# Kernel tuning notes

Measured on AMD Instinct MI355X. Metric: run time of the kernel, lower is better.

Reference implementation:

```python
import jax, jax.numpy as jnp
import jax.scipy.linalg as jsl
import numpy as np

B, T, C = 2, 4096, 1024
HK = HV = 8           # linear_num_key_heads == linear_num_value_heads
DK = DV = 128         # linear_key_head_dim / linear_value_head_dim
CHUNK = 64
CONV_K = 4
KEY_DIM = HK * DK
VAL_DIM = HV * DV
CONV_DIM = 2 * KEY_DIM + VAL_DIM
EPS = 1e-6


def setup_inputs() -> dict:
    key = jax.random.key(0)
    ks = jax.random.split(key, 8)
    s = 0.02
    x = jax.random.normal(ks[0], (B, T, C), jnp.float32)
    W_qkvz = jax.random.normal(ks[1], (C, 2 * KEY_DIM + 2 * VAL_DIM), jnp.float32) * s
    W_ba = jax.random.normal(ks[2], (C, 2 * HV), jnp.float32) * s
    conv_w = jax.random.normal(ks[3], (CONV_DIM, 1, CONV_K), jnp.float32) * 0.3  # depthwise (O,1,K)
    dt_bias = jnp.ones((HV,), jnp.float32)
    A_log = jnp.log(jax.random.uniform(ks[4], (HV,), jnp.float32, 0.5, 8.0))
    norm_weight = jnp.ones((DV,), jnp.float32)
    W_out = jax.random.normal(ks[5], (VAL_DIM, C), jnp.float32) * s
    return {"x": x, "W_qkvz": W_qkvz, "W_ba": W_ba, "conv_w": conv_w,
            "dt_bias": dt_bias, "A_log": A_log, "norm_weight": norm_weight, "W_out": W_out}


def _l2norm(x, eps=EPS):
    return x * jax.lax.rsqrt(jnp.sum(x * x, -1, keepdims=True) + eps)


def _chunk_gated_delta_rule(q, k, v, g, beta, chunk=CHUNK):
    # q,k: (B,T,H,DK); v: (B,T,H,DV); g,beta: (B,T,H)
    q = _l2norm(q)
    k = _l2norm(k)
    tr = lambda x: jnp.swapaxes(x, 1, 2).astype(jnp.float32)  # -> (B,H,T,...)
    q, k, v, g, beta = tr(q), tr(k), tr(v), tr(g), tr(beta)
    b, h, t, dk = k.shape
    dv = v.shape[-1]
    n = t // chunk  # T divisible by chunk (pad_size == 0)
    q = q * (dk ** -0.5)
    v_beta = v * beta[..., None]
    k_beta = k * beta[..., None]
    rs = lambda x: x.reshape(b, h, n, chunk, x.shape[-1])
    q, k, v_beta, k_beta = rs(q), rs(k), rs(v_beta), rs(k_beta)
    g = jnp.cumsum(g.reshape(b, h, n, chunk), axis=-1)
    # decay_mask[..., i, j] = exp(g_i - g_j) for j <= i, else 0
    decay = jnp.tril(jnp.exp(jnp.tril(g[..., :, None] - g[..., None, :])))
    # forward substitution == unit-lower-triangular solve: (I + tri)^{-1}
    tri = jnp.tril(jnp.einsum('bhnck,bhndk->bhncd', k_beta, k) * decay, -1)
    eye = jnp.eye(chunk, dtype=jnp.float32)
    Tm = jsl.solve_triangular(eye + tri, jnp.broadcast_to(eye, tri.shape), lower=True)
    v_new = Tm @ v_beta                                   # (B,H,N,C,DV)
    k_cum = Tm @ (k_beta * jnp.exp(g)[..., None])         # (B,H,N,C,DK)
    keep_low = jnp.tril(jnp.ones((chunk, chunk), bool))

    def step(S, inp):
        q_i, k_i, v_i, kc_i, g_i, dm_i = inp              # (B,H,C,*)
        attn = jnp.where(keep_low, (q_i @ jnp.swapaxes(k_i, -1, -2)) * dm_i, 0.0)
        v_n = v_i - kc_i @ S
        out = (q_i * jnp.exp(g_i)[..., None]) @ S + attn @ v_n
        g_last = g_i[..., -1]
        S = S * jnp.exp(g_last)[..., None, None] + jnp.einsum(
            'bhck,bhcv->bhkv', k_i * jnp.exp(g_last[..., None] - g_i)[..., None], v_n)
        return S, out

    mv = lambda x: jnp.moveaxis(x, 2, 0)                  # chunk axis to front
    S0 = jnp.zeros((b, h, dk, dv), jnp.float32)
    S, outs = jax.lax.scan(step, S0, (mv(q), mv(k), mv(v_new), mv(k_cum), mv(g), mv(decay)))
    out = jnp.moveaxis(outs, 0, 2).reshape(b, h, t, dv)
    return jnp.swapaxes(out, 1, 2), S                     # (B,T,H,DV), (B,H,DK,DV)


def reference(x, W_qkvz, W_ba, conv_w, dt_bias, A_log, norm_weight, W_out):
    Bx, Tx, Cx = x.shape
    ratio = HV // HK
    qkvz = (x @ W_qkvz).reshape(Bx, Tx, HK, 2 * DK + 2 * ratio * DV)
    q, k, v, z = jnp.split(qkvz, [DK, 2 * DK, 2 * DK + ratio * DV], axis=3)
    v = v.reshape(Bx, Tx, HV, DV)
    z = z.reshape(Bx, Tx, HV, DV)
    ba = (x @ W_ba).reshape(Bx, Tx, HK, 2 * ratio)
    b_, a_ = jnp.split(ba, [ratio], axis=3)
    b_ = b_.reshape(Bx, Tx, HV)
    a_ = a_.reshape(Bx, Tx, HV)
    mixed = jnp.concatenate([q.reshape(Bx, Tx, -1), k.reshape(Bx, Tx, -1),
                             v.reshape(Bx, Tx, -1)], axis=-1)
    # causal depthwise conv1d (left pad K-1, take first T)
    xc = jnp.swapaxes(mixed, 1, 2)                        # (B, CONV_DIM, T)
    conv = jax.lax.conv_general_dilated(xc, conv_w, (1,), [(CONV_K - 1, 0)],
                                        dimension_numbers=('NCH', 'OIH', 'NCH'),
                                        feature_group_count=CONV_DIM)
    conv = jnp.swapaxes(jax.nn.silu(conv), 1, 2)          # (B,T,CONV_DIM)
    qc, kc, vc = jnp.split(conv, [KEY_DIM, 2 * KEY_DIM], axis=-1)
    qc = qc.reshape(Bx, Tx, HK, DK)
    kc = kc.reshape(Bx, Tx, HK, DK)
    vc = vc.reshape(Bx, Tx, HV, DV)
    if ratio > 1:
        qc = jnp.repeat(qc, ratio, axis=2)
        kc = jnp.repeat(kc, ratio, axis=2)
    beta = jax.nn.sigmoid(b_)
    g = -jnp.exp(A_log) * jax.nn.softplus(a_ + dt_bias)
    core, _ = _chunk_gated_delta_rule(qc, kc, vc, g, beta)
    # GatedRMSNorm over head_v_dim, gated by silu(z)
    h = core.astype(jnp.float32)
    var = jnp.mean(h * h, -1, keepdims=True)
    h = norm_weight * (h * jax.lax.rsqrt(var + EPS))
    h = h * jax.nn.silu(z.astype(jnp.float32))
    return h.reshape(Bx, Tx, VAL_DIM) @ W_out
```

## Files before the change

kernel.cpp:

```cpp
#include <hip/hip_runtime.h>
#include <cstddef>

#define Bx 2
#define Tn 4096
#define Hh 8

typedef unsigned short u16;
typedef unsigned int u32;
typedef __attribute__((ext_vector_type(8))) short short8;
typedef __attribute__((ext_vector_type(4))) float f32x4;

__device__ __forceinline__ float bf2f(u16 u) {
  u32 x = ((u32)u) << 16;
  return __uint_as_float(x);
}
__device__ __forceinline__ u16 f2bf(float f) {
  u32 x = __float_as_uint(f);
  u32 lsb = (x >> 16) & 1;
  x += 0x7fffu + lsb;
  return (u16)(x >> 16);
}
__device__ __forceinline__ u32 pack2(float a, float b) {
  return (u32)f2bf(a) | ((u32)f2bf(b) << 16);
}
__device__ __forceinline__ short8 cvt8(float4 f0, float4 f1) {
  uint4 p;
  p.x = pack2(f0.x, f0.y);
  p.y = pack2(f0.z, f0.w);
  p.z = pack2(f1.x, f1.y);
  p.w = pack2(f1.z, f1.w);
  return *(short8*)&p;
}
__device__ __forceinline__ void async16(u16* lds, const u16* g) {
  __builtin_amdgcn_global_load_lds((const __attribute__((address_space(1))) void*)g,
                                   (__attribute__((address_space(3))) void*)lds, 16, 0, 0);
}

__global__ __launch_bounds__(256) void conv_bf16(const float* __restrict__ X,
                                                 u16* __restrict__ Xb) {
  int i = (blockIdx.x * 256 + threadIdx.x) * 8;
  float4 v0 = *(const float4*)&X[i];
  float4 v1 = *(const float4*)&X[i + 4];
  uint4 pv;
  pv.x = pack2(v0.x, v0.y);
  pv.y = pack2(v0.z, v0.w);
  pv.z = pack2(v1.x, v1.y);
  pv.w = pack2(v1.z, v1.w);
  *(uint4*)&Xb[i] = pv;
}

__global__ __launch_bounds__(256) void transpose_bf16(const float* __restrict__ W,
                                                      u16* __restrict__ WT,
                                                      int K, int N) {
  __shared__ float tile[64][68];
  int nb = blockIdx.x, kb = blockIdx.y;
  int tid = threadIdx.x;
  int r = tid >> 4, c4 = (tid & 15) * 4;
#pragma unroll
  for (int p = 0; p < 4; p++) {
    int k = kb * 64 + p * 16 + r;
    float4 v = *(const float4*)&W[(size_t)k * N + nb * 64 + c4];
    tile[p * 16 + r][c4] = v.x;
    tile[p * 16 + r][c4 + 1] = v.y;
    tile[p * 16 + r][c4 + 2] = v.z;
    tile[p * 16 + r][c4 + 3] = v.w;
  }
  __syncthreads();
  int rn = tid >> 2, ck = (tid & 3) * 16;
#pragma unroll
  for (int s = 0; s < 2; s++) {
    int k0 = ck + s * 8;
    uint4 pv;
    pv.x = pack2(tile[k0 + 0][rn], tile[k0 + 1][rn]);
    pv.y = pack2(tile[k0 + 2][rn], tile[k0 + 3][rn]);
    pv.z = pack2(tile[k0 + 4][rn], tile[k0 + 5][rn]);
    pv.w = pack2(tile[k0 + 6][rn], tile[k0 + 7][rn]);
    *(uint4*)&WT[(size_t)(nb * 64 + rn) * K + kb * 64 + k0] = pv;
  }
}

template<int EPI>
__global__ __launch_bounds__(256) void gemm_mfma(const u16* __restrict__ A,
                                                 const u16* __restrict__ Bt,
                                                 u16* __restrict__ O1,
                                                 u16* __restrict__ O2,
                                                 float* __restrict__ O3,
                                                 int Nfull) {
  const int K = 1024;
  __shared__ u16 As[128 * 32];
  __shared__ u16 Bs[128 * 32];
  int bn = blockIdx.x, bm = blockIdx.y;
  int tid = threadIdx.x;
  int wave = tid >> 6, lane = tid & 63;
  int wr = wave >> 1, wc = wave & 1;

  f32x4 acc[4][4];
#pragma unroll
  for (int i = 0; i < 4; i++)
#pragma unroll
    for (int j = 0; j < 4; j++) acc[i][j] = (f32x4){0.f, 0.f, 0.f, 0.f};

  const u16* Ab = A + (size_t)(bm * 128 + wave * 32 + (lane >> 2)) * K + (lane & 3) * 8;
  const u16* Bb = Bt + (size_t)(bn * 128 + wave * 32 + (lane >> 2)) * K + (lane & 3) * 8;
  u16* AsW = &As[(wave * 32) * 32];
  u16* BsW = &Bs[(wave * 32) * 32];

  int m_lane = lane & 15, k_lane = (lane >> 4) * 8;
  const u16* arow0 = &As[(wr * 64 + m_lane) * 32 + k_lane];
  const u16* brow0 = &Bs[(wc * 64 + m_lane) * 32 + k_lane];

  for (int kk = 0; kk < K; kk += 32) {
    __syncthreads();
    async16(AsW, Ab + kk);
    async16(AsW + 16 * 32, Ab + 16 * K + kk);
    async16(BsW, Bb + kk);
    async16(BsW + 16 * 32, Bb + 16 * K + kk);
    __syncthreads();
    short8 a[4], b[4];
#pragma unroll
    for (int t = 0; t < 4; t++) a[t] = *(const short8*)(arow0 + t * 16 * 32);
#pragma unroll
    for (int t = 0; t < 4; t++) b[t] = *(const short8*)(brow0 + t * 16 * 32);
#pragma unroll
    for (int i = 0; i < 4; i++)
#pragma unroll
      for (int j = 0; j < 4; j++)
        acc[i][j] = __builtin_amdgcn_mfma_f32_16x16x32_bf16(a[i], b[j], acc[i][j], 0, 0, 0);
  }

  int n0 = bn * 128;
  int cbase = wc * 64 + (lane & 15);
  int rbase = bm * 128 + wr * 64 + ((lane >> 4) * 4);
  if (EPI == 1) {
    int h = n0 >> 9, sub = (n0 >> 7) & 3;
    u16* dst;
    size_t stride;
    if (sub < 3) { dst = O1 + (size_t)(sub * 1024 + h * 128); stride = 3072; }
    else         { dst = O2 + (size_t)(h * 128);              stride = 1024; }
#pragma unroll
    for (int i = 0; i < 4; i++)
#pragma unroll
      for (int j = 0; j < 4; j++)
#pragma unroll
        for (int r = 0; r < 4; r++)
          dst[(size_t)(rbase + i * 16 + r) * stride + cbase + j * 16] = f2bf(acc[i][j][r]);
  } else {
#pragma unroll
    for (int i = 0; i < 4; i++)
#pragma unroll
      for (int j = 0; j < 4; j++)
#pragma unroll
        for (int r = 0; r < 4; r++)
          O3[(size_t)(rbase + i * 16 + r) * Nfull + n0 + cbase + j * 16] = acc[i][j][r];
  }
}

__global__ __launch_bounds__(128) void ba_kernel(const float* __restrict__ x,
                                                 const float* __restrict__ Wba,
                                                 const float* __restrict__ dtb,
                                                 const float* __restrict__ Alog,
                                                 float* __restrict__ betab,
                                                 float* __restrict__ gb) {
  __shared__ float xs[1024];
  __shared__ float part[8][16];
  int row = blockIdx.x, tid = threadIdx.x;
#pragma unroll
  for (int r = 0; r < 2; r++) {
    int f4 = r * 128 + tid;
    *(float4*)&xs[f4 * 4] = *(const float4*)&x[(size_t)row * 1024 + f4 * 4];
  }
  __syncthreads();
  int col = tid & 15, seg = tid >> 4;
  float a = 0.f;
  for (int k = seg * 128; k < seg * 128 + 128; k++) a += xs[k] * Wba[k * 16 + col];
  part[seg][col] = a;
  __syncthreads();
  if (tid < 8) {
    float bval = 0.f, aval = 0.f;
#pragma unroll
    for (int q = 0; q < 8; q++) { bval += part[q][tid * 2]; aval += part[q][tid * 2 + 1]; }
    betab[(size_t)row * 8 + tid] = 1.f / (1.f + expf(-bval));
    float spin = aval + dtb[tid];
    float sp = (spin > 20.f) ? spin : log1pf(expf(spin));
    gb[(size_t)row * 8 + tid] = -expf(Alog[tid]) * sp;
  }
}

__global__ __launch_bounds__(256) void convnorm(const u16* __restrict__ mixed,
                                                const float* __restrict__ cw,
                                                const float* __restrict__ gbuf,
                                                u16* __restrict__ qn,
                                                u16* __restrict__ kn,
                                                u16* __restrict__ kdT) {
  __shared__ __align__(16) u16 sRaw[67 * 128];
  __shared__ __align__(16) u16 sO[64 * 136];
  __shared__ float red_s[256];
  __shared__ float inv_s[64];
  __shared__ float eglc_s[64];
  int n = blockIdx.x, bh = blockIdx.y, type = blockIdx.z;
  int b = bh >> 3, h = bh & 7;
  int t0 = n * 64, tid = threadIdx.x;
  int srow = tid >> 4, scol8 = (tid & 15) * 8;
  int base = type * 1024;

#pragma unroll
  for (int pass = 0; pass < 5; pass++) {
    int r = pass * 16 + srow;
    if (r < 67) {
      int t = t0 - 3 + r;
      uint4 v = make_uint4(0u, 0u, 0u, 0u);
      if (t >= 0) v = *(const uint4*)&mixed[(size_t)(b * Tn + t) * 3072 + base + h * 128 + scol8];
      *(uint4*)&sRaw[r * 128 + scol8] = v;
    }
  }
  if (type == 1 && tid < 64) {
    float gv = gbuf[(size_t)(b * Tn + t0 + tid) * 8 + h];
#pragma unroll
    for (int off = 1; off < 64; off <<= 1) {
      float o = __shfl_up(gv, off, 64);
      if (tid >= off) gv += o;
    }
    float gl = __shfl(gv, 63, 64);
    eglc_s[tid] = expf(gl - gv);
  }
  __syncthreads();

#pragma unroll
  for (int it = 0; it < 32; it++) {
    int idx = it * 256 + tid;
    int i = idx >> 7, d = idx & 127;
    int colw = (base + h * 128 + d) * 4;
    float a = 0.f;
#pragma unroll
    for (int tap = 0; tap < 4; tap++)
      a += bf2f(sRaw[(i + tap) * 128 + d]) * cw[colw + tap];
    a = a / (1.f + expf(-a));
    sO[i * 136 + d] = f2bf(a);
  }
  __syncthreads();
  {
    int i = tid >> 2, p = tid & 3;
    float ss = 0.f;
#pragma unroll
    for (int d = p * 32; d < p * 32 + 32; d += 2) {
      u32 w2 = *(const u32*)&sO[i * 136 + d];
      float a = bf2f(w2 & 0xffff), b2 = bf2f(w2 >> 16);
      ss += a * a + b2 * b2;
    }
    red_s[tid] = ss;
  }
  __syncthreads();
  if (tid < 64) {
    float inv = rsqrtf(red_s[tid * 4] + red_s[tid * 4 + 1] + red_s[tid * 4 + 2] + red_s[tid * 4 + 3] + 1e-6f);
    inv_s[tid] = (type == 0) ? inv * 0.08838834764831845f : inv;
  }
  __syncthreads();
  u16* dstRow = (type == 0 ? qn : kn) + (size_t)(bh * Tn + t0) * 128;
#pragma unroll
  for (int it = 0; it < 16; it++) {
    int idx = it * 256 + tid;
    int i = idx >> 6, d2 = (idx & 63) * 2;
    u32 w2 = *(const u32*)&sO[i * 136 + d2];
    float inv = inv_s[i];
    float q0 = bf2f(w2 & 0xffff) * inv, q1 = bf2f(w2 >> 16) * inv;
    u32 pk = pack2(q0, q1);
    if (type == 1) *(u32*)&sO[i * 136 + d2] = pk;
    *(u32*)&dstRow[(size_t)i * 128 + d2] = pk;
  }
  if (type == 1) {
    __syncthreads();
    const size_t tbase = (size_t)(bh * 64 + n) * 8192;
#pragma unroll
    for (int it = 0; it < 32; it++) {
      int idx = it * 256 + tid;
      int d = idx >> 6, i = idx & 63;
      kdT[tbase + d * 64 + i] = f2bf(bf2f(sO[i * 136 + d]) * eglc_s[i]);
    }
  }
}

__global__ __launch_bounds__(256) void prep(const u16* __restrict__ mixed,
                                            const float* __restrict__ cw,
                                            const float* __restrict__ gbuf,
                                            const float* __restrict__ betabuf,
                                            u16* qbuf,
                                            u16* kbuf,
                                            u16* __restrict__ vnT,
                                            u16* __restrict__ attn,
                                            float* __restrict__ egl) {
  __shared__ __align__(16) u16 sKn[64 * 136];
  __shared__ __align__(16) u16 sQn[64 * 136];
  __shared__ __align__(16) u16 sRawV[67 * 128];
  __shared__ float gc_s[64], egc_s[64], bet_s[64];
  float* triL = (float*)sQn;

  int n = blockIdx.x, bh = blockIdx.y;
  int b = bh >> 3, h = bh & 7;
  int t0 = n * 64;
  int tid = threadIdx.x;
  const int rowg0 = b * Tn + t0;
  const int rowh0 = bh * Tn + t0;
  const size_t tbase = (size_t)(bh * 64 + n) * 8192;

  int wv = tid >> 6, lane = tid & 63;
  int m16 = lane & 15, q8 = (lane >> 4) * 8, qr = (lane >> 4) * 4;
  int srow = tid >> 4, scol8 = (tid & 15) * 8;

#pragma unroll
  for (int it = 0; it < 4; it++) {
    int idx = it * 256 + tid;
    int i = idx >> 4, c8 = (idx & 15) * 8;
    *(uint4*)&sQn[i * 136 + c8] = *(const uint4*)&qbuf[(size_t)(rowh0 + i) * 128 + c8];
    *(uint4*)&sKn[i * 136 + c8] = *(const uint4*)&kbuf[(size_t)(rowh0 + i) * 128 + c8];
  }
#pragma unroll
  for (int pass = 0; pass < 5; pass++) {
    int r = pass * 16 + srow;
    if (r < 67) {
      int t = t0 - 3 + r;
      uint4 v = make_uint4(0u, 0u, 0u, 0u);
      if (t >= 0) v = *(const uint4*)&mixed[(size_t)(b * Tn + t) * 3072 + 2048 + h * 128 + scol8];
      *(uint4*)&sRawV[r * 128 + scol8] = v;
    }
  }
  if (tid < 64) {
    float gv = gbuf[(size_t)(rowg0 + tid) * 8 + h];
    float bv = betabuf[(size_t)(rowg0 + tid) * 8 + h];
#pragma unroll
    for (int off = 1; off < 64; off <<= 1) {
      float o = __shfl_up(gv, off, 64);
      if (tid >= off) gv += o;
    }
    float gl = __shfl(gv, 63, 64);
    gc_s[tid] = gv;
    egc_s[tid] = expf(gv);
    bet_s[tid] = bv;
    if (tid == 63) egl[bh * 64 + n] = expf(gl);
  }
  __syncthreads();

#pragma unroll
  for (int it = 0; it < 16; it++) {
    int idx = it * 256 + tid;
    int i = idx >> 6, d2 = (idx & 63) * 2;
    u32 w2 = *(const u32*)&sQn[i * 136 + d2];
    float e = egc_s[i];
    *(u32*)&qbuf[(size_t)(rowh0 + i) * 128 + d2] =
        pack2(bf2f(w2 & 0xffff) * e, bf2f(w2 >> 16) * e);
  }
  {
    short8 qa[4];
#pragma unroll
    for (int kt = 0; kt < 4; kt++)
      qa[kt] = *(const short8*)&sQn[(wv * 16 + m16) * 136 + kt * 32 + q8];
    u16* atp = attn + (size_t)(bh * 64 + n) * 4096;
#pragma unroll
    for (int jt = 0; jt < 4; jt++) {
      int j = jt * 16 + m16;
      if (jt <= wv) {
        f32x4 o = (f32x4){0.f, 0.f, 0.f, 0.f};
#pragma unroll
        for (int kt = 0; kt < 4; kt++) {
          short8 kb = *(const short8*)&sKn[(jt * 16 + m16) * 136 + kt * 32 + q8];
          o = __builtin_amdgcn_mfma_f32_16x16x32_bf16(qa[kt], kb, o, 0, 0, 0);
        }
#pragma unroll
        for (int r = 0; r < 4; r++) {
          int i = wv * 16 + qr + r;
          float val = (j <= i) ? o[r] * expf(gc_s[i] - gc_s[j]) : 0.f;
          atp[i * 64 + j] = f2bf(val);
        }
      } else {
#pragma unroll
        for (int r = 0; r < 4; r++) atp[(wv * 16 + qr + r) * 64 + j] = 0;
      }
    }
  }
  __syncthreads();
  {
    short8 ka[4];
#pragma unroll
    for (int kt = 0; kt < 4; kt++)
      ka[kt] = *(const short8*)&sKn[(wv * 16 + m16) * 136 + kt * 32 + q8];
#pragma unroll
    for (int jt = 0; jt < 4; jt++) {
      int j = jt * 16 + m16;
      if (jt <= wv) {
        f32x4 o = (f32x4){0.f, 0.f, 0.f, 0.f};
#pragma unroll
        for (int kt = 0; kt < 4; kt++) {
          short8 kb = *(const short8*)&sKn[(jt * 16 + m16) * 136 + kt * 32 + q8];
          o = __builtin_amdgcn_mfma_f32_16x16x32_bf16(ka[kt], kb, o, 0, 0, 0);
        }
#pragma unroll
        for (int r = 0; r < 4; r++) {
          int i = wv * 16 + qr + r;
          triL[i * 64 + j] = (j < i) ? bet_s[i] * expf(gc_s[i] - gc_s[j]) * o[r] : 0.f;
        }
      } else if (jt == wv + 1) {
#pragma unroll
        for (int r = 0; r < 4; r++) triL[(wv * 16 + qr + r) * 64 + j] = 0.f;
      }
    }
  }
  __syncthreads();

  {
    int mat = tid >> 7, c = tid & 127;
    float x[64];
    if (mat == 0) {
#pragma unroll
      for (int i = 0; i < 64; i++)
        x[i] = bf2f(sKn[i * 136 + c]) * bet_s[i] * egc_s[i];
    } else {
      float cwv[4];
      int colw = (2048 + h * 128 + c) * 4;
#pragma unroll
      for (int tap = 0; tap < 4; tap++) cwv[tap] = cw[colw + tap];
#pragma unroll
      for (int i = 0; i < 64; i++) {
        float a = 0.f;
#pragma unroll
        for (int tap = 0; tap < 4; tap++)
          a += bf2f(sRawV[(i + tap) * 128 + c]) * cwv[tap];
        a = a / (1.f + expf(-a));
        x[i] = a * bet_s[i];
      }
    }
#pragma unroll
    for (int i = 1; i < 64; i++) {
      float s0 = 0.f, s1 = 0.f, s2 = 0.f, s3 = 0.f;
#pragma unroll
      for (int l4 = 0; l4 < (i + 3) / 4; l4++) {
        float4 t4 = *(float4*)&triL[i * 64 + l4 * 4];
        s0 += t4.x * x[l4 * 4 + 0];
        s1 += t4.y * x[l4 * 4 + 1];
        s2 += t4.z * x[l4 * 4 + 2];
        s3 += t4.w * x[l4 * 4 + 3];
      }
      x[i] = x[i] - ((s0 + s1) + (s2 + s3));
    }
    if (mat == 0) {
#pragma unroll
      for (int i = 0; i < 64; i++) kbuf[(size_t)(rowh0 + i) * 128 + c] = f2bf(-x[i]);
    } else {
#pragma unroll
      for (int i = 0; i < 64; i += 2)
        *(u32*)&vnT[tbase + c * 64 + i] = pack2(x[i], x[i + 1]);
    }
  }
}

__device__ __forceinline__ void stage_quarter(int w, u16* ldsb,
                                              const u16* __restrict__ qgc,
                                              const u16* __restrict__ kcc,
                                              const u16* __restrict__ ktc,
                                              const u16* __restrict__ atc,
                                              const u16* __restrict__ vtc,
                                              int lane) {
  int l8 = lane * 8;
  if (w == 0) {
#pragma unroll
    for (int i = 0; i < 16; i++) {
      int p = i * 512 + l8;
      async16(ldsb + 8192 + i * 512, kcc + (p ^ ((((p >> 7) & 15)) << 3)));
    }
  } else if (w == 1) {
#pragma unroll
    for (int i = 0; i < 16; i++) {
      int p = i * 512 + l8;
      async16(ldsb + 16384 + i * 512, ktc + (p ^ ((((p >> 6) & 7)) << 3)));
    }
  } else if (w == 2) {
#pragma unroll
    for (int i = 0; i < 16; i++) {
      int p = i * 512 + l8;
      async16(ldsb + i * 512, qgc + (p ^ ((((p >> 7) & 15)) << 3)));
    }
  } else {
#pragma unroll
    for (int i = 0; i < 8; i++) {
      int p = i * 512 + l8;
      async16(ldsb + 24576 + i * 512, atc + (p ^ ((((p >> 6) & 7)) << 3)));
    }
#pragma unroll
    for (int i = 0; i < 2; i++) {
      int p = i * 512 + l8;
      async16(ldsb + 28672 + i * 512, vtc + (p ^ ((((p >> 6) & 7)) << 3)));
    }
  }
}

__global__ __launch_bounds__(256, 1) void scan_mfma(const u16* __restrict__ qg,
                                                    const u16* __restrict__ kdT,
                                                    const u16* __restrict__ vnT,
                                                    const u16* __restrict__ kcum,
                                                    const u16* __restrict__ attn,
                                                    const float* __restrict__ egl,
                                                    float* __restrict__ core) {
  extern __shared__ __align__(16) u16 dyn[];
  __shared__ __align__(16) u16 STb[16 * 128];
  __shared__ __align__(16) u16 VNb[16 * 64];
  int blk = blockIdx.x;
  int bh = blk & 15, tile = blk >> 4;
  int dv0 = tile * 16;
  int b = bh >> 3, h = bh & 7;
  int tid = threadIdx.x;
  int w = tid >> 6, lane = tid & 63;
  int q = lane >> 4, col = lane & 15;
  int c7 = col & 7;
  int qh = q >> 1, ql = q & 1;

  for (int r = tid; r < 16 * 128 / 2; r += 256) ((u32*)STb)[r] = 0u;
  float egAll = egl[bh * 64 + lane];

  f32x4 st0 = (f32x4){0.f, 0.f, 0.f, 0.f};
  f32x4 st1 = (f32x4){0.f, 0.f, 0.f, 0.f};

  const u16* qg_base = qg + (size_t)bh * Tn * 128;
  const u16* kc_base = kcum + (size_t)bh * Tn * 128;
  const u16* kt_base = kdT + (size_t)bh * 64 * 8192;
  const u16* at_base = attn + (size_t)bh * 64 * 4096;
  const u16* vt_base = vnT + (size_t)bh * 64 * 8192 + dv0 * 64;

  stage_quarter(w, dyn, qg_base, kc_base, kt_base, at_base, vt_base, lane);
  asm volatile("s_waitcnt vmcnt(0)" ::: "memory");
  __syncthreads();

  for (int n = 0; n < 64; n++) {
    u16* buf = dyn + (n & 1) * 29696;

    short8 kcf[4], qgf[4], ktf[4], atf[2], sb[4];
    uint2 vtf;
#pragma unroll
    for (int kt = 0; kt < 4; kt++) {
      kcf[kt] = *(const short8*)&buf[8192 + (w * 16 + col) * 128 + (((kt * 4 + q) ^ col) << 3)];
      qgf[kt] = *(const short8*)&buf[(w * 16 + col) * 128 + (((kt * 4 + q) ^ col) << 3)];
      sb[kt] = *(const short8*)&STb[col * 128 + (((kt * 4 + q) ^ col) << 3)];
    }
#pragma unroll
    for (int kt2 = 0; kt2 < 2; kt2++) {
      atf[kt2] = *(const short8*)&buf[24576 + (w * 16 + col) * 64 + (((kt2 * 4 + q) ^ c7) << 3)];
#pragma unroll
      for (int t = 0; t < 2; t++)
        ktf[t * 2 + kt2] = *(const short8*)&buf[16384 + ((w * 2 + t) * 16 + col) * 64 +
                                                (((kt2 * 4 + q) ^ c7) << 3)];
    }
    vtf = *(const uint2*)&buf[28672 + col * 64 + (((w * 2 + qh) ^ c7) << 3) + ql * 4];

    if (n < 63) {
      stage_quarter(w, dyn + ((n + 1) & 1) * 29696,
                    qg_base + (size_t)(n + 1) * 8192,
                    kc_base + (size_t)(n + 1) * 8192,
                    kt_base + (size_t)(n + 1) * 8192,
                    at_base + (size_t)(n + 1) * 4096,
                    vt_base + (size_t)(n + 1) * 8192, lane);
    }
    float eg = __shfl(egAll, n, 64);

    {
      f32x4 a0;
      a0[0] = bf2f(vtf.x & 0xffff); a0[1] = bf2f(vtf.x >> 16);
      a0[2] = bf2f(vtf.y & 0xffff); a0[3] = bf2f(vtf.y >> 16);
#pragma unroll
      for (int kt = 0; kt < 4; kt++)
        a0 = __builtin_amdgcn_mfma_f32_16x16x32_bf16(kcf[kt], sb[kt], a0, 0, 0, 0);
      uint2 pk;
      pk.x = pack2(a0[0], a0[1]);
      pk.y = pack2(a0[2], a0[3]);
      *(uint2*)&VNb[col * 64 + (((w * 2 + qh) ^ c7) << 3) + ql * 4] = pk;
    }
    asm volatile("s_waitcnt lgkmcnt(0)" ::: "memory");
    __builtin_amdgcn_s_barrier();
    __builtin_amdgcn_sched_barrier(0);

    short8 vb[2];
#pragma unroll
    for (int kt2 = 0; kt2 < 2; kt2++)
      vb[kt2] = *(const short8*)&VNb[col * 64 + (((kt2 * 4 + q) ^ c7) << 3)];

    {
      f32x4 s0;
      s0[0] = st0[0] * eg; s0[1] = st0[1] * eg; s0[2] = st0[2] * eg; s0[3] = st0[3] * eg;
      s0 = __builtin_amdgcn_mfma_f32_16x16x32_bf16(ktf[0], vb[0], s0, 0, 0, 0);
      s0 = __builtin_amdgcn_mfma_f32_16x16x32_bf16(ktf[1], vb[1], s0, 0, 0, 0);
      st0 = s0;
      uint2 pk;
      pk.x = pack2(s0[0], s0[1]);
      pk.y = pack2(s0[2], s0[3]);
      *(uint2*)&STb[col * 128 + ((((w * 2 + 0) * 2 + qh) ^ col) << 3) + ql * 4] = pk;
    }
    {
      f32x4 s1;
      s1[0] = st1[0] * eg; s1[1] = st1[1] * eg; s1[2] = st1[2] * eg; s1[3] = st1[3] * eg;
      s1 = __builtin_amdgcn_mfma_f32_16x16x32_bf16(ktf[2], vb[0], s1, 0, 0, 0);
      s1 = __builtin_amdgcn_mfma_f32_16x16x32_bf16(ktf[3], vb[1], s1, 0, 0, 0);
      st1 = s1;
      uint2 pk;
      pk.x = pack2(s1[0], s1[1]);
      pk.y = pack2(s1[2], s1[3]);
      *(uint2*)&STb[col * 128 + ((((w * 2 + 1) * 2 + qh) ^ col) << 3) + ql * 4] = pk;
    }

    {
      f32x4 o = (f32x4){0.f, 0.f, 0.f, 0.f};
#pragma unroll
      for (int kt = 0; kt < 4; kt++)
        o = __builtin_amdgcn_mfma_f32_16x16x32_bf16(qgf[kt], sb[kt], o, 0, 0, 0);
#pragma unroll
      for (int kt2 = 0; kt2 < 2; kt2++)
        o = __builtin_amdgcn_mfma_f32_16x16x32_bf16(atf[kt2], vb[kt2], o, 0, 0, 0);
      size_t rowb = (size_t)(b * Tn) + n * 64 + w * 16 + q * 4;
#pragma unroll
      for (int r2 = 0; r2 < 4; r2++)
        core[(rowb + r2) * 1024 + h * 128 + dv0 + col] = o[r2];
    }

    asm volatile("s_waitcnt vmcnt(4) lgkmcnt(0)" ::: "memory");
    __builtin_amdgcn_s_barrier();
    __builtin_amdgcn_sched_barrier(0);
  }
}

__global__ __launch_bounds__(256) void gnorm(const float* __restrict__ core,
                                             const u16* __restrict__ z,
                                             const float* __restrict__ nw,
                                             u16* __restrict__ coreb) {
  __shared__ float red[256];
  __shared__ float rstd[8];
  int row = blockIdx.x, tid = threadIdx.x;
  float4 c4 = *(const float4*)&core[(size_t)row * 1024 + tid * 4];
  uint2 zl = *(const uint2*)&z[(size_t)row * 1024 + tid * 4];
  float4 z4;
  z4.x = bf2f(zl.x & 0xffff); z4.y = bf2f(zl.x >> 16);
  z4.z = bf2f(zl.y & 0xffff); z4.w = bf2f(zl.y >> 16);
  red[tid] = c4.x * c4.x + c4.y * c4.y + c4.z * c4.z + c4.w * c4.w;
  __syncthreads();
  if (tid < 8) {
    float s = 0.f;
    for (int t2 = tid * 32; t2 < tid * 32 + 32; t2++) s += red[t2];
    rstd[tid] = rsqrtf(s * (1.f / 128.f) + 1e-6f);
  }
  __syncthreads();
  float rs = rstd[tid >> 5];
  int d0 = (tid * 4) & 127;
  float4 w4 = *(const float4*)&nw[d0];
  float4 o;
  o.x = c4.x * rs * w4.x * (z4.x / (1.f + expf(-z4.x)));
  o.y = c4.y * rs * w4.y * (z4.y / (1.f + expf(-z4.y)));
  o.z = c4.z * rs * w4.z * (z4.z / (1.f + expf(-z4.z)));
  o.w = c4.w * rs * w4.w * (z4.w / (1.f + expf(-z4.w)));
  uint2 pv;
  pv.x = pack2(o.x, o.y);
  pv.y = pack2(o.z, o.w);
  *(uint2*)&coreb[(size_t)row * 1024 + tid * 4] = pv;
}

extern "C" void kernel_launch(void* const* d_in, const int* in_sizes, int n_in,
                              void* d_out, int out_size, void* d_ws, size_t ws_size,
                              hipStream_t stream) {
  const float* x     = (const float*)d_in[0];
  const float* Wqkvz = (const float*)d_in[1];
  const float* Wba   = (const float*)d_in[2];
  const float* convw = (const float*)d_in[3];
  const float* dtb   = (const float*)d_in[4];
  const float* Alog  = (const float*)d_in[5];
  const float* nw    = (const float*)d_in[6];
  const float* Wout  = (const float*)d_in[7];
  float* out = (float*)d_out;

  char* w = (char*)d_ws;
  u16*   mixed = (u16*)w;
  float* core  = (float*)w;
  u16*   coreb = (u16*)(w + 33554432);
  u16*   zb    = (u16*)(w + 50331648);
  float* betab = (float*)(w + 67108864);
  float* gb    = (float*)(w + 67371008);
  u16*   qgB   = (u16*)(w + 67633152);
  u16*   xb    = (u16*)(w + 67633152);
  u16*   kdTB  = (u16*)(w + 84410368);
  u16*   WqT   = (u16*)(w + 84410368);
  u16*   vnTB  = (u16*)(w + 101187584);
  u16*   kcB   = (u16*)(w + 117964800);
  u16*   WoT   = (u16*)(w + 117964800);
  u16*   atB   = (u16*)(w + 134742016);
  float* eglB  = (float*)(w + 143130624);

  static bool attr_set = false;
  if (!attr_set) {
    hipFuncSetAttribute(reinterpret_cast<const void*>(scan_mfma),
                        hipFuncAttributeMaxDynamicSharedMemorySize, 118784);
    attr_set = true;
  }

  conv_bf16<<<dim3(4096), 256, 0, stream>>>(x, xb);
  transpose_bf16<<<dim3(64, 16), 256, 0, stream>>>(Wqkvz, WqT, 1024, 4096);
  gemm_mfma<1><<<dim3(32, 64), 256, 0, stream>>>(xb, WqT, mixed, zb, nullptr, 4096);
  ba_kernel<<<dim3(8192), 128, 0, stream>>>(x, Wba, dtb, Alog, betab, gb);
  convnorm<<<dim3(64, 16, 2), 256, 0, stream>>>(mixed, convw, gb, qgB, kcB, kdTB);
  prep<<<dim3(64, 16), 256, 0, stream>>>(mixed, convw, gb, betab, qgB, kcB, vnTB, atB, eglB);
  scan_mfma<<<dim3(128), 256, 118784, stream>>>(qgB, kdTB, vnTB, kcB, atB, eglB, core);
  transpose_bf16<<<dim3(16, 16), 256, 0, stream>>>(Wout, WoT, 1024, 1024);
  gnorm<<<dim3(8192), 256, 0, stream>>>(core, zb, nw, coreb);
  gemm_mfma<0><<<dim3(8, 64), 256, 0, stream>>>(coreb, WoT, nullptr, nullptr, out, 1024);
}
```

Before: 418.6 us.

## Double GEMM K-tile to 64 with XOR-swizzled LDS and block remapping

The bf16 MFMA GEMM now stages a 64-wide K slice per iteration instead of 32. This halves the number of barrier pairs and doubles the MFMA work between syncs. LDS rows are XOR-swizzled on both the async store and the fragment loads to avoid bank conflicts with the wider 128-byte rows. Block indices are remapped so groups of eight consecutive blocks spread across N columns, aiming at better L2 locality. LDS use doubles and the remap assumes gridDim.x is divisible by 8.

```diff
diff --git a/kernel.cpp b/kernel.cpp
--- a/kernel.cpp
+++ b/kernel.cpp
@@ -87,9 +87,13 @@
                                                  float* __restrict__ O3,
                                                  int Nfull) {
   const int K = 1024;
-  __shared__ u16 As[128 * 32];
-  __shared__ u16 Bs[128 * 32];
-  int bn = blockIdx.x, bm = blockIdx.y;
+  __shared__ u16 As[128 * 64];
+  __shared__ u16 Bs[128 * 64];
+  int lin = blockIdx.y * gridDim.x + blockIdx.x;
+  int sl = lin >> 3;
+  int cbn = gridDim.x >> 3;
+  int bn = (lin & 7) * cbn + (sl % cbn);
+  int bm = sl / cbn;
   int tid = threadIdx.x;
   int wave = tid >> 6, lane = tid & 63;
   int wr = wave >> 1, wc = wave & 1;
@@ -100,32 +104,42 @@
 #pragma unroll
     for (int j = 0; j < 4; j++) acc[i][j] = (f32x4){0.f, 0.f, 0.f, 0.f};
 
-  const u16* Ab = A + (size_t)(bm * 128 + wave * 32 + (lane >> 2)) * K + (lane & 3) * 8;
-  const u16* Bb = Bt + (size_t)(bn * 128 + wave * 32 + (lane >> 2)) * K + (lane & 3) * 8;
-  u16* AsW = &As[(wave * 32) * 32];
-  u16* BsW = &Bs[(wave * 32) * 32];
-
-  int m_lane = lane & 15, k_lane = (lane >> 4) * 8;
-  const u16* arow0 = &As[(wr * 64 + m_lane) * 32 + k_lane];
-  const u16* brow0 = &Bs[(wc * 64 + m_lane) * 32 + k_lane];
-
-  for (int kk = 0; kk < K; kk += 32) {
+  int srow = lane >> 3;
+  int gc8 = ((lane & 7) ^ srow) * 8;
+  const u16* Ab = A + (size_t)(bm * 128 + wave * 32 + srow) * K + gc8;
+  const u16* Bb = Bt + (size_t)(bn * 128 + wave * 32 + srow) * K + gc8;
+  u16* AsW = &As[(wave * 32) * 64];
+  u16* BsW = &Bs[(wave * 32) * 64];
+
+  int m_lane = lane & 15, kgrp = lane >> 4;
+  int m7 = m_lane & 7;
+
+  for (int kk = 0; kk < K; kk += 64) {
     __syncthreads();
-    async16(AsW, Ab + kk);
-    async16(AsW + 16 * 32, Ab + 16 * K + kk);
-    async16(BsW, Bb + kk);
-    async16(BsW + 16 * 32, Bb + 16 * K + kk);
+#pragma unroll
+    for (int i = 0; i < 4; i++) {
+      async16(AsW + i * 512, Ab + (size_t)(i * 8) * K + kk);
+      async16(BsW + i * 512, Bb + (size_t)(i * 8) * K + kk);
+    }
     __syncthreads();
-    short8 a[4], b[4];
-#pragma unroll
-    for (int t = 0; t < 4; t++) a[t] = *(const short8*)(arow0 + t * 16 * 32);
-#pragma unroll
-    for (int t = 0; t < 4; t++) b[t] = *(const short8*)(brow0 + t * 16 * 32);
-#pragma unroll
-    for (int i = 0; i < 4; i++)
-#pragma unroll
-      for (int j = 0; j < 4; j++)
-        acc[i][j] = __builtin_amdgcn_mfma_f32_16x16x32_bf16(a[i], b[j], acc[i][j], 0, 0, 0);
+    short8 a[4][2], b[4][2];
+#pragma unroll
+    for (int t = 0; t < 4; t++)
+#pragma unroll
+      for (int ks = 0; ks < 2; ks++) {
+        a[t][ks] = *(const short8*)&As[(wr * 64 + t * 16 + m_lane) * 64 +
+                                       (((ks * 4 + kgrp) ^ m7) << 3)];
+        b[t][ks] = *(const short8*)&Bs[(wc * 64 + t * 16 + m_lane) * 64 +
+                                       (((ks * 4 + kgrp) ^ m7) << 3)];
+      }
+#pragma unroll
+    for (int ks = 0; ks < 2; ks++)
+#pragma unroll
+      for (int i = 0; i < 4; i++)
+#pragma unroll
+        for (int j = 0; j < 4; j++)
+          acc[i][j] = __builtin_amdgcn_mfma_f32_16x16x32_bf16(a[i][ks], b[j][ks],
+                                                              acc[i][j], 0, 0, 0);
   }
 
   int n0 = bn * 128;
```

New measurement: 400.3 us. 1.05x faster.
